# Optimization experiments

Measured on AMD Instinct MI355X. Metric: run time of the kernel, lower is better.

## Reference

```python
import jax, jax.numpy as jnp
import numpy as np

N_NODES = 100000
N_EDGES = 1600000
N_GRAPHS = 64
IN_DIM = 397


def setup_inputs() -> dict:
    key = jax.random.key(0)
    ks = jax.random.split(key, 16)
    x = jax.random.normal(ks[0], (N_NODES, IN_DIM), dtype=jnp.float32)
    edge_index = jax.random.randint(ks[1], (2, N_EDGES), 0, N_NODES, dtype=jnp.int64)
    batch = jnp.sort(jax.random.randint(ks[2], (N_NODES,), 0, N_GRAPHS, dtype=jnp.int64))

    def lin(k, fan_in, fan_out):
        s = 1.0 / np.sqrt(fan_in)
        return jax.random.uniform(k, (fan_in, fan_out), jnp.float32, -s, s)

    return {
        "x": x, "edge_index": edge_index, "batch": batch,
        "W1": lin(ks[3], IN_DIM, 128), "b1": jnp.zeros((128,), jnp.float32),
        "W2": lin(ks[4], 128, 128),   "b2": jnp.zeros((128,), jnp.float32),
        "W3": lin(ks[5], 128, 64),    "b3": jnp.zeros((64,), jnp.float32),
        "Wh1": lin(ks[6], 64, 32),    "bh1": jnp.zeros((32,), jnp.float32),
        "Wh2": lin(ks[7], 32, 1),     "bh2": jnp.zeros((1,), jnp.float32),
    }


def _gcn_conv(x, src, dst, deg_isqrt, W, b, n_nodes):
    # PyG GCNConv: linear first, then sym-normalized aggregation with self-loops.
    xw = x @ W  # [N, out]
    norm = deg_isqrt[src] * deg_isqrt[dst]  # [E]
    agg = jax.ops.segment_sum(xw[src] * norm[:, None], dst, num_segments=n_nodes)
    # self-loop contribution: deg^{-1/2}[i] * deg^{-1/2}[i] * xw[i]
    agg = agg + xw * (deg_isqrt * deg_isqrt)[:, None]
    return agg + b


def reference(x, edge_index, batch, W1, b1, W2, b2, W3, b3, Wh1, bh1, Wh2, bh2):
    n_nodes = x.shape[0]
    src, dst = edge_index[0], edge_index[1]
    # degree after adding self-loops (edge weight 1), counted at destination
    deg = jax.ops.segment_sum(jnp.ones_like(src, dtype=x.dtype), dst,
                              num_segments=n_nodes) + 1.0
    deg_isqrt = jax.lax.rsqrt(deg)

    h = jax.nn.relu(_gcn_conv(x, src, dst, deg_isqrt, W1, b1, n_nodes))
    # dropout p=0.2 -> identity in eval
    h = jax.nn.relu(_gcn_conv(h, src, dst, deg_isqrt, W2, b2, n_nodes))
    h = jax.nn.relu(_gcn_conv(h, src, dst, deg_isqrt, W3, b3, n_nodes))

    # global max pool over graphs in the batch
    g = jax.ops.segment_max(h, batch, num_segments=N_GRAPHS)  # [G, 64]

    # MLP head (Dropout(0.3) identity in eval)
    g = jax.nn.relu(g @ Wh1 + bh1)
    out = g @ Wh2 + bh2  # [G, 1]
    return out.squeeze(-1)
```

## Files before the change

### kernel.cpp

```cpp
#include <hip/hip_runtime.h>
#include <hip/hip_bf16.h>
#include <hip/hip_fp16.h>


typedef float f4u __attribute__((ext_vector_type(4), aligned(4)));
typedef unsigned short u16;
typedef u16 u16x8 __attribute__((ext_vector_type(8)));
typedef short bf16x8 __attribute__((ext_vector_type(8)));
typedef float f32x4 __attribute__((ext_vector_type(4)));
typedef _Float16 f16;
typedef f16 f16x8 __attribute__((ext_vector_type(8)));

__device__ __forceinline__ u16 bf16_rne(float f) {
    unsigned u = __float_as_uint(f);
    return (u16)((u + 0x7FFF + ((u >> 16) & 1)) >> 16);
}
__device__ __forceinline__ float bf16_f(u16 h) {
    return __uint_as_float(((unsigned)h) << 16);
}

__global__ void deg_count_kernel(const int* __restrict__ ei, int* __restrict__ cnt, int E) {
    int e = blockIdx.x * 256 + threadIdx.x;
    if (e < E) atomicAdd(&cnt[ei[E + e]], 1);
}

__global__ void deg_fin_kernel(const int* __restrict__ cnt, float* __restrict__ disq, int N) {
    int i = blockIdx.x * 256 + threadIdx.x;
    if (i < N) disq[i] = rsqrtf((float)cnt[i] + 1.0f);
}

__global__ void scan_pass1(const int* __restrict__ cnt, int* __restrict__ bsum, int N) {
    __shared__ int s[256];
    int t = threadIdx.x;
    int base = blockIdx.x * 1024 + t * 4;
    int sum = 0;
    #pragma unroll
    for (int j = 0; j < 4; ++j) { int idx = base + j; if (idx < N) sum += cnt[idx]; }
    s[t] = sum; __syncthreads();
    for (int off = 128; off; off >>= 1) {
        if (t < off) s[t] += s[t + off];
        __syncthreads();
    }
    if (t == 0) bsum[blockIdx.x] = s[0];
}

__global__ void scan_pass2(const int* __restrict__ bsum, int* __restrict__ boff,
                           int nchunks, int* __restrict__ rp, int N, int E) {
    __shared__ int s[256];
    int t = threadIdx.x;
    int v = (t < nchunks) ? bsum[t] : 0;
    s[t] = v; __syncthreads();
    for (int off = 1; off < 256; off <<= 1) {
        int x = (t >= off) ? s[t - off] : 0;
        __syncthreads();
        s[t] += x;
        __syncthreads();
    }
    boff[t] = s[t] - v;
    if (t == 0) rp[N] = E;
}

__global__ void scan_pass3(const int* __restrict__ cnt, const int* __restrict__ boff,
                           int* __restrict__ rp, int N) {
    __shared__ int s[256];
    int t = threadIdx.x;
    int base = blockIdx.x * 1024 + t * 4;
    int v[4]; int sum = 0;
    #pragma unroll
    for (int j = 0; j < 4; ++j) { int idx = base + j; v[j] = (idx < N) ? cnt[idx] : 0; sum += v[j]; }
    s[t] = sum; __syncthreads();
    for (int off = 1; off < 256; off <<= 1) {
        int x = (t >= off) ? s[t - off] : 0;
        __syncthreads();
        s[t] += x;
        __syncthreads();
    }
    int ex = s[t] - sum + boff[blockIdx.x];
    #pragma unroll
    for (int j = 0; j < 4; ++j) { int idx = base + j; if (idx < N) { rp[idx] = ex; ex += v[j]; } }
}

__global__ void scatter_kernel(const int* __restrict__ ei, const float* __restrict__ disq,
                               const int* __restrict__ rp, int* __restrict__ fill,
                               int2* __restrict__ esw, int E) {
    int e = blockIdx.x * 256 + threadIdx.x;
    if (e >= E) return;
    int s = ei[e];
    int d = ei[E + e];
    int pos = rp[d] + atomicAdd(&fill[d], 1);
    int2 p; p.x = s; p.y = __float_as_int(disq[s] * disq[d]);
    esw[pos] = p;
}

template <int BN>
__global__ void cvtw_kernel(const float* __restrict__ W, u16* __restrict__ Wfhi,
                            u16* __restrict__ Wflo, int K, int KP) {
    constexpr int FC = BN / 16;
    int idx = blockIdx.x * 256 + threadIdx.x;
    if (idx >= KP * BN) return;
    int j = idx & 7;
    int u = (idx >> 3) & 63;
    int tf = idx >> 9;
    int fc = tf % FC;
    int t = tf / FC;
    int c = fc * 16 + (u >> 2);
    int k = t * 32 + (u & 3) * 8 + j;
    float v = (k < K) ? W[(long)k * BN + c] : 0.f;
    u16 h = bf16_rne(v);
    Wfhi[idx] = h;
    Wflo[idx] = bf16_rne(v - bf16_f(h));
}

template <int BN, bool AFP32>
__global__ __launch_bounds__(512) void mfma_gemm(
    const float* __restrict__ Af, const u16* __restrict__ Ahi,
    const u16* __restrict__ Alo, const u16* __restrict__ Wfhi,
    const u16* __restrict__ Wflo, f16* __restrict__ Xh, int N, int K, int KP)
{
    constexpr int FC = BN / 16;
    constexpr int PLANE = BN * 32;
    __shared__ u16 Wlds[2 * PLANE];
    const int tid = threadIdx.x;
    const int w = tid >> 6;
    const int l = tid & 63;
    const int l15 = l & 15;
    const int g = l >> 4;
    const int koff = g * 8;
    const long base = (long)blockIdx.x * 128;
    const long arow = base + w * 16 + l15;
    const bool rowOK = (arow < N);
    const int bro = (l15 * 4 + g) * 8;

    f32x4 acc[FC];
    #pragma unroll
    for (int j = 0; j < FC; ++j) acc[j] = (f32x4){0.f, 0.f, 0.f, 0.f};

    const int T = KP / 32;
    for (int t = 0; t < T; ++t) {
        if (BN == 128 || tid < PLANE / 8) {
            const u16* gph = Wfhi + (long)t * PLANE + tid * 8;
            const u16* gpl = Wflo + (long)t * PLANE + tid * 8;
            __builtin_amdgcn_global_load_lds(
                (const __attribute__((address_space(1))) void*)gph,
                (__attribute__((address_space(3))) void*)((char*)Wlds + w * 1024), 16, 0, 0);
            __builtin_amdgcn_global_load_lds(
                (const __attribute__((address_space(1))) void*)gpl,
                (__attribute__((address_space(3))) void*)((char*)Wlds + PLANE * 2 + w * 1024), 16, 0, 0);
        }
        const int k0 = t * 32;
        bf16x8 ah, al;
        {
            u16x8 hv = (u16x8)0, lv = (u16x8)0;
            if constexpr (AFP32) {
                int rem = K - (k0 + koff);
                if (rowOK && rem > 0) {
                    const float* ap = &Af[arow * (long)K + k0 + koff];
                    float f[8];
                    if (rem >= 8) {
                        f4u v0 = *(const f4u*)ap;
                        f4u v1 = *(const f4u*)(ap + 4);
                        f[0] = v0.x; f[1] = v0.y; f[2] = v0.z; f[3] = v0.w;
                        f[4] = v1.x; f[5] = v1.y; f[6] = v1.z; f[7] = v1.w;
                    } else {
                        #pragma unroll
                        for (int j = 0; j < 8; ++j) f[j] = (j < rem) ? ap[j] : 0.f;
                    }
                    #pragma unroll
                    for (int j = 0; j < 8; ++j) {
                        u16 h = bf16_rne(f[j]);
                        hv[j] = h;
                        lv[j] = bf16_rne(f[j] - bf16_f(h));
                    }
                }
            } else {
                if (rowOK) {
                    hv = *(const u16x8*)&Ahi[arow * (long)K + k0 + koff];
                    lv = *(const u16x8*)&Alo[arow * (long)K + k0 + koff];
                }
            }
            ah = __builtin_bit_cast(bf16x8, hv);
            al = __builtin_bit_cast(bf16x8, lv);
        }
        __syncthreads();
        #pragma unroll
        for (int fc = 0; fc < FC; ++fc) {
            bf16x8 bh = *(const bf16x8*)&Wlds[fc * 512 + bro];
            bf16x8 bl = *(const bf16x8*)&Wlds[PLANE + fc * 512 + bro];
            acc[fc] = __builtin_amdgcn_mfma_f32_16x16x32_bf16(ah, bh, acc[fc], 0, 0, 0);
            acc[fc] = __builtin_amdgcn_mfma_f32_16x16x32_bf16(al, bh, acc[fc], 0, 0, 0);
            acc[fc] = __builtin_amdgcn_mfma_f32_16x16x32_bf16(ah, bl, acc[fc], 0, 0, 0);
        }
        __syncthreads();
    }
    #pragma unroll
    for (int fc = 0; fc < FC; ++fc) {
        int col = fc * 16 + l15;
        #pragma unroll
        for (int reg = 0; reg < 4; ++reg) {
            long row = base + w * 16 + g * 4 + reg;
            if (row < N) Xh[row * BN + col] = (f16)acc[fc][reg];
        }
    }
}

template <int C, bool B16OUT>
__global__ __launch_bounds__(256) void agg_kernel(
    const f16* __restrict__ xh, const float* __restrict__ disq,
    const int* __restrict__ rp, const int2* __restrict__ esw,
    const float* __restrict__ bias, float* __restrict__ h,
    u16* __restrict__ hhi, u16* __restrict__ hlo, int N)
{
    int i = blockIdx.x * 4 + (threadIdx.x >> 6);
    if (i >= N) return;
    int lane = threadIdx.x & 63;
    int e0 = rp[i], e1 = rp[i + 1];
    constexpr int LPE = C / 8;
    constexpr int EPW = 64 / LPE;
    int sub = lane / LPE;
    int col = lane % LPE;
    const f16x8* x8 = (const f16x8*)xh;

    float a0[8], a1[8];
    #pragma unroll
    for (int j = 0; j < 8; ++j) { a0[j] = 0.f; a1[j] = 0.f; }

    int e = e0 + sub;
    for (; e + EPW < e1; e += 2 * EPW) {
        int2 p0 = esw[e];
        int2 p1 = esw[e + EPW];
        f16x8 v0 = x8[(long)p0.x * LPE + col];
        f16x8 v1 = x8[(long)p1.x * LPE + col];
        float w0 = __int_as_float(p0.y), w1 = __int_as_float(p1.y);
        #pragma unroll
        for (int j = 0; j < 8; ++j) {
            a0[j] += (float)v0[j] * w0;
            a1[j] += (float)v1[j] * w1;
        }
    }
    for (; e < e1; e += EPW) {
        int2 p0 = esw[e];
        f16x8 v0 = x8[(long)p0.x * LPE + col];
        float w0 = __int_as_float(p0.y);
        #pragma unroll
        for (int j = 0; j < 8; ++j) a0[j] += (float)v0[j] * w0;
    }
    #pragma unroll
    for (int j = 0; j < 8; ++j) a0[j] += a1[j];
    #pragma unroll
    for (int m = LPE; m < 64; m <<= 1) {
        #pragma unroll
        for (int j = 0; j < 8; ++j) a0[j] += __shfl_xor(a0[j], m, 64);
    }
    if (sub == 0) {
        float ds = disq[i];
        float ws = ds * ds;
        f16x8 v = x8[(long)i * LPE + col];
        const float* bp = bias + col * 8;
        float4 b0 = *(const float4*)bp;
        float4 b1 = *(const float4*)(bp + 4);
        float bb[8] = {b0.x, b0.y, b0.z, b0.w, b1.x, b1.y, b1.z, b1.w};
        float o[8];
        #pragma unroll
        for (int j = 0; j < 8; ++j)
            o[j] = fmaxf(a0[j] + (float)v[j] * ws + bb[j], 0.f);
        if constexpr (B16OUT) {
            u16x8 oh, ol;
            #pragma unroll
            for (int j = 0; j < 8; ++j) {
                u16 hh = bf16_rne(o[j]);
                oh[j] = hh;
                ol[j] = bf16_rne(o[j] - bf16_f(hh));
            }
            *(u16x8*)&hhi[(long)i * C + col * 8] = oh;
            *(u16x8*)&hlo[(long)i * C + col * 8] = ol;
        } else {
            float4 v0 = {o[0], o[1], o[2], o[3]};
            float4 v1 = {o[4], o[5], o[6], o[7]};
            *(float4*)&h[(long)i * C + col * 8] = v0;
            *(float4*)&h[(long)i * C + col * 8 + 4] = v1;
        }
    }
}

__global__ __launch_bounds__(256) void pool_kernel(
    const float* __restrict__ h, const int* __restrict__ batch,
    float* __restrict__ g, int N)
{
    int c = threadIdx.x & 63;
    int slot = threadIdx.x >> 6;
    int base = blockIdx.x * 512;
    int end = base + 512; if (end > N) end = N;
    int cur = -1; float m = 0.f;
    for (int n = base + slot; n < end; n += 4) {
        int b = batch[n];
        float v = h[(long)n * 64 + c];
        if (b != cur) {
            if (cur >= 0) atomicMax((int*)&g[cur * 64 + c], __float_as_int(m));
            cur = b; m = v;
        } else {
            m = fmaxf(m, v);
        }
    }
    if (cur >= 0) atomicMax((int*)&g[cur * 64 + c], __float_as_int(m));
}

__global__ void head_kernel(const float* __restrict__ g, const float* __restrict__ Wh1,
                            const float* __restrict__ bh1, const float* __restrict__ Wh2,
                            const float* __restrict__ bh2, float* __restrict__ out, int G) {
    int r = threadIdx.x;
    if (r >= G) return;
    float hid[32];
    #pragma unroll
    for (int j = 0; j < 32; ++j) {
        float s = bh1[j];
        for (int k = 0; k < 64; ++k) s += g[r * 64 + k] * Wh1[k * 32 + j];
        hid[j] = fmaxf(s, 0.f);
    }
    float o = bh2[0];
    #pragma unroll
    for (int j = 0; j < 32; ++j) o += hid[j] * Wh2[j];
    out[r] = o;
}

extern "C" void kernel_launch(void* const* d_in, const int* in_sizes, int n_in,
                              void* d_out, int out_size, void* d_ws, size_t ws_size,
                              hipStream_t stream) {
    const float* x   = (const float*)d_in[0];
    const int*   ei  = (const int*)d_in[1];
    const int*   bat = (const int*)d_in[2];
    const float* W1  = (const float*)d_in[3];
    const float* b1  = (const float*)d_in[4];
    const float* W2  = (const float*)d_in[5];
    const float* b2  = (const float*)d_in[6];
    const float* W3  = (const float*)d_in[7];
    const float* b3  = (const float*)d_in[8];
    const float* Wh1 = (const float*)d_in[9];
    const float* bh1 = (const float*)d_in[10];
    const float* Wh2 = (const float*)d_in[11];
    const float* bh2 = (const float*)d_in[12];
    float* out = (float*)d_out;

    const int N = in_sizes[2];
    const int E = in_sizes[1] / 2;
    const int K1 = in_sizes[0] / N;
    const int G = out_size;
    const int KP1 = ((K1 + 31) / 32) * 32;

    char* wsp = (char*)d_ws;
    size_t off = 0;
    auto alloc = [&](size_t bytes) -> void* {
        void* p = wsp + off;
        off = (off + bytes + 255) & ~(size_t)255;
        return p;
    };
    int*   cnt   = (int*)alloc((size_t)N * 4);
    float* disq  = (float*)alloc((size_t)N * 4);
    int*   rp    = (int*)alloc((size_t)(N + 1) * 4);
    int*   bsum  = (int*)alloc(256 * 4);
    int*   boff  = (int*)alloc(256 * 4);
    int2*  esw   = (int2*)alloc((size_t)E * 8);
    u16*   Wf1hi = (u16*)alloc((size_t)KP1 * 128 * 2);
    u16*   Wf1lo = (u16*)alloc((size_t)KP1 * 128 * 2);
    u16*   Wf2hi = (u16*)alloc((size_t)128 * 128 * 2);
    u16*   Wf2lo = (u16*)alloc((size_t)128 * 128 * 2);
    u16*   Wf3hi = (u16*)alloc((size_t)128 * 64 * 2);
    u16*   Wf3lo = (u16*)alloc((size_t)128 * 64 * 2);
    f16*   Xh    = (f16*)alloc((size_t)N * 128 * 2);
    u16*   Hhi   = (u16*)alloc((size_t)N * 128 * 2);
    u16*   Hlo   = (u16*)alloc((size_t)N * 128 * 2);
    float* h3    = (float*)alloc((size_t)N * 64 * 4);
    float* g     = (float*)alloc((size_t)G * 64 * 4);

    const int nchunks = (N + 1023) / 1024;

    (void)hipMemsetAsync(cnt, 0, (size_t)N * 4, stream);
    deg_count_kernel<<<(E + 255) / 256, 256, 0, stream>>>(ei, cnt, E);
    deg_fin_kernel<<<(N + 255) / 256, 256, 0, stream>>>(cnt, disq, N);
    scan_pass1<<<nchunks, 256, 0, stream>>>(cnt, bsum, N);
    scan_pass2<<<1, 256, 0, stream>>>(bsum, boff, nchunks, rp, N, E);
    scan_pass3<<<nchunks, 256, 0, stream>>>(cnt, boff, rp, N);
    (void)hipMemsetAsync(cnt, 0, (size_t)N * 4, stream);
    scatter_kernel<<<(E + 255) / 256, 256, 0, stream>>>(ei, disq, rp, cnt, esw, E);

    cvtw_kernel<128><<<(KP1 * 128 + 255) / 256, 256, 0, stream>>>(W1, Wf1hi, Wf1lo, K1, KP1);
    cvtw_kernel<128><<<(128 * 128 + 255) / 256, 256, 0, stream>>>(W2, Wf2hi, Wf2lo, 128, 128);
    cvtw_kernel<64><<<(128 * 64 + 255) / 256, 256, 0, stream>>>(W3, Wf3hi, Wf3lo, 128, 128);

    int gblocks = (N + 127) / 128;
    int ablocks = (N + 3) / 4;
    mfma_gemm<128, true><<<gblocks, 512, 0, stream>>>(x, nullptr, nullptr, Wf1hi, Wf1lo, Xh, N, K1, KP1);
    agg_kernel<128, true><<<ablocks, 256, 0, stream>>>(Xh, disq, rp, esw, b1, nullptr, Hhi, Hlo, N);
    mfma_gemm<128, false><<<gblocks, 512, 0, stream>>>(nullptr, Hhi, Hlo, Wf2hi, Wf2lo, Xh, N, 128, 128);
    agg_kernel<128, true><<<ablocks, 256, 0, stream>>>(Xh, disq, rp, esw, b2, nullptr, Hhi, Hlo, N);
    mfma_gemm<64, false><<<gblocks, 512, 0, stream>>>(nullptr, Hhi, Hlo, Wf3hi, Wf3lo, Xh, N, 128, 128);
    agg_kernel<64, false><<<ablocks, 256, 0, stream>>>(Xh, disq, rp, esw, b3, h3, nullptr, nullptr, N);
    (void)hipMemsetAsync(g, 0, (size_t)G * 64 * 4, stream);
    pool_kernel<<<(N + 511) / 512, 256, 0, stream>>>(h3, bat, g, N);
    head_kernel<<<1, 64, 0, stream>>>(g, Wh1, bh1, Wh2, bh2, out, G);
}
```

Before: 529.9 us.

## Double-buffer weight tiles in LDS and prefetch next A fragment in GEMM

The MFMA GEMM now keeps two LDS buffers for the weight tiles. It issues the global-to-LDS load for step t+1 before the MFMAs of step t and prefetches the next A fragment into registers, which removes one __syncthreads per iteration. The weight pre-conversion layout is also changed so each lane reads a contiguous 16-byte chunk at l*8, which is meant to make LDS reads conflict-free. The cost is twice the LDS footprint and extra registers for the prefetched A, which could lower occupancy.

```diff
diff --git a/kernel.cpp b/kernel.cpp
--- a/kernel.cpp
+++ b/kernel.cpp
@@ -99,12 +99,12 @@
     int idx = blockIdx.x * 256 + threadIdx.x;
     if (idx >= KP * BN) return;
     int j = idx & 7;
-    int u = (idx >> 3) & 63;
+    int s = (idx >> 3) & 63;
     int tf = idx >> 9;
     int fc = tf % FC;
     int t = tf / FC;
-    int c = fc * 16 + (u >> 2);
-    int k = t * 32 + (u & 3) * 8 + j;
+    int c = fc * 16 + (s & 15);
+    int k = t * 32 + ((s >> 4) & 3) * 8 + j;
     float v = (k < K) ? W[(long)k * BN + c] : 0.f;
     u16 h = bf16_rne(v);
     Wfhi[idx] = h;
@@ -119,7 +119,7 @@
 {
     constexpr int FC = BN / 16;
     constexpr int PLANE = BN * 32;
-    __shared__ u16 Wlds[2 * PLANE];
+    __shared__ u16 Wlds[2][2 * PLANE];
     const int tid = threadIdx.x;
     const int w = tid >> 6;
     const int l = tid & 63;
@@ -129,68 +129,80 @@
     const long base = (long)blockIdx.x * 128;
     const long arow = base + w * 16 + l15;
     const bool rowOK = (arow < N);
-    const int bro = (l15 * 4 + g) * 8;
+    const int bro = l * 8;
 
     f32x4 acc[FC];
     #pragma unroll
     for (int j = 0; j < FC; ++j) acc[j] = (f32x4){0.f, 0.f, 0.f, 0.f};
 
-    const int T = KP / 32;
-    for (int t = 0; t < T; ++t) {
+    auto stageW = [&](int t, int buf) {
         if (BN == 128 || tid < PLANE / 8) {
             const u16* gph = Wfhi + (long)t * PLANE + tid * 8;
             const u16* gpl = Wflo + (long)t * PLANE + tid * 8;
             __builtin_amdgcn_global_load_lds(
                 (const __attribute__((address_space(1))) void*)gph,
-                (__attribute__((address_space(3))) void*)((char*)Wlds + w * 1024), 16, 0, 0);
+                (__attribute__((address_space(3))) void*)((char*)&Wlds[buf][0] + w * 1024), 16, 0, 0);
             __builtin_amdgcn_global_load_lds(
                 (const __attribute__((address_space(1))) void*)gpl,
-                (__attribute__((address_space(3))) void*)((char*)Wlds + PLANE * 2 + w * 1024), 16, 0, 0);
-        }
+                (__attribute__((address_space(3))) void*)((char*)&Wlds[buf][PLANE] + w * 1024), 16, 0, 0);
+        }
+    };
+    auto loadA = [&](int t, bf16x8& ah, bf16x8& al) {
         const int k0 = t * 32;
-        bf16x8 ah, al;
-        {
-            u16x8 hv = (u16x8)0, lv = (u16x8)0;
-            if constexpr (AFP32) {
-                int rem = K - (k0 + koff);
-                if (rowOK && rem > 0) {
-                    const float* ap = &Af[arow * (long)K + k0 + koff];
-                    float f[8];
-                    if (rem >= 8) {
-                        f4u v0 = *(const f4u*)ap;
-                        f4u v1 = *(const f4u*)(ap + 4);
-                        f[0] = v0.x; f[1] = v0.y; f[2] = v0.z; f[3] = v0.w;
-                        f[4] = v1.x; f[5] = v1.y; f[6] = v1.z; f[7] = v1.w;
-                    } else {
-                        #pragma unroll
-                        for (int j = 0; j < 8; ++j) f[j] = (j < rem) ? ap[j] : 0.f;
-                    }
+        u16x8 hv = (u16x8)0, lv = (u16x8)0;
+        if constexpr (AFP32) {
+            int rem = K - (k0 + koff);
+            if (rowOK && rem > 0) {
+                const float* ap = &Af[arow * (long)K + k0 + koff];
+                float f[8];
+                if (rem >= 8) {
+                    f4u v0 = *(const f4u*)ap;
+                    f4u v1 = *(const f4u*)(ap + 4);
+                    f[0] = v0.x; f[1] = v0.y; f[2] = v0.z; f[3] = v0.w;
+                    f[4] = v1.x; f[5] = v1.y; f[6] = v1.z; f[7] = v1.w;
+                } else {
                     #pragma unroll
-                    for (int j = 0; j < 8; ++j) {
-                        u16 h = bf16_rne(f[j]);
-                        hv[j] = h;
-                        lv[j] = bf16_rne(f[j] - bf16_f(h));
-                    }
+                    for (int j = 0; j < 8; ++j) f[j] = (j < rem) ? ap[j] : 0.f;
                 }
-            } else {
-                if (rowOK) {
-                    hv = *(const u16x8*)&Ahi[arow * (long)K + k0 + koff];
-                    lv = *(const u16x8*)&Alo[arow * (long)K + k0 + koff];
+                #pragma unroll
+                for (int j = 0; j < 8; ++j) {
+                    u16 h = bf16_rne(f[j]);
+                    hv[j] = h;
+                    lv[j] = bf16_rne(f[j] - bf16_f(h));
                 }
             }
-            ah = __builtin_bit_cast(bf16x8, hv);
-            al = __builtin_bit_cast(bf16x8, lv);
-        }
-        __syncthreads();
+        } else {
+            if (rowOK) {
+                hv = *(const u16x8*)&Ahi[arow * (long)K + k0 + koff];
+                lv = *(const u16x8*)&Alo[arow * (long)K + k0 + koff];
+            }
+        }
+        ah = __builtin_bit_cast(bf16x8, hv);
+        al = __builtin_bit_cast(bf16x8, lv);
+    };
+
+    const int T = KP / 32;
+    bf16x8 ahC, alC, ahN, alN;
+    stageW(0, 0);
+    loadA(0, ahC, alC);
+    __syncthreads();
+
+    for (int t = 0; t < T; ++t) {
+        const int buf = t & 1;
+        const bool more = (t + 1 < T);
+        if (more) stageW(t + 1, buf ^ 1);
+        if (!AFP32 && more) loadA(t + 1, ahN, alN);
         #pragma unroll
         for (int fc = 0; fc < FC; ++fc) {
-            bf16x8 bh = *(const bf16x8*)&Wlds[fc * 512 + bro];
-            bf16x8 bl = *(const bf16x8*)&Wlds[PLANE + fc * 512 + bro];
-            acc[fc] = __builtin_amdgcn_mfma_f32_16x16x32_bf16(ah, bh, acc[fc], 0, 0, 0);
-            acc[fc] = __builtin_amdgcn_mfma_f32_16x16x32_bf16(al, bh, acc[fc], 0, 0, 0);
-            acc[fc] = __builtin_amdgcn_mfma_f32_16x16x32_bf16(ah, bl, acc[fc], 0, 0, 0);
-        }
-        __syncthreads();
+            bf16x8 bh = *(const bf16x8*)&Wlds[buf][fc * 512 + bro];
+            bf16x8 bl = *(const bf16x8*)&Wlds[buf][PLANE + fc * 512 + bro];
+            acc[fc] = __builtin_amdgcn_mfma_f32_16x16x32_bf16(ahC, bh, acc[fc], 0, 0, 0);
+            acc[fc] = __builtin_amdgcn_mfma_f32_16x16x32_bf16(alC, bh, acc[fc], 0, 0, 0);
+            acc[fc] = __builtin_amdgcn_mfma_f32_16x16x32_bf16(ahC, bl, acc[fc], 0, 0, 0);
+        }
+        if (AFP32 && more) loadA(t + 1, ahN, alN);
+        __syncthreads();
+        ahC = ahN; alC = alN;
     }
     #pragma unroll
     for (int fc = 0; fc < FC; ++fc) {
```

Result: no change. 521.7 us (-1.5%).
